# Optimization experiments

Measured on AMD Instinct MI355X. Metric: run time of the kernel, lower is better.

The kernel has to match this reference:

```python
import jax, jax.numpy as jnp
import numpy as np

B, N, D, OUT = 8, 2048, 128, 128

def setup_inputs() -> dict:
    key = jax.random.key(0)
    k1, k2, k3, k4 = jax.random.split(key, 4)
    input_ = jax.random.normal(k1, (B, N, D), dtype=jnp.float32)
    adj_matrix = jax.random.randint(k2, (B, N, N), 0, 2, dtype=jnp.int32)
    W = jax.random.normal(k3, (2 * D, OUT), dtype=jnp.float32) * 0.05
    b = jax.random.normal(k4, (OUT,), dtype=jnp.float32) * 0.05
    return {"input_": input_, "adj_matrix": adj_matrix, "W": W, "b": b}

def reference(input_, adj_matrix, W, b):
    adj = adj_matrix.astype(jnp.float32)           # [B,N,N]
    deg = jnp.sum(adj, axis=2)                     # [B,N]
    deg = jnp.where(deg == 0, 1.0, deg)
    agg = jnp.einsum('bnm,bmd->bnd', adj, input_) / deg[:, :, None]  # mean aggregation
    feat = jnp.concatenate([input_, agg], axis=2)  # [B,N,2D]
    out = jax.nn.sigmoid(feat @ W + b)             # [B,N,OUT]
    out = out / jnp.linalg.norm(out, axis=2, keepdims=True)
    return out
```

## Files before the change

kernel.cpp:

```cpp
#include <hip/hip_runtime.h>

#define Bn 8
#define Nn 2048
#define Dn 128
#define OUTn 128

typedef __attribute__((ext_vector_type(8))) short bf16x8;
typedef __attribute__((ext_vector_type(8))) unsigned short ushort8;
typedef __attribute__((ext_vector_type(4))) float f32x4;
typedef __attribute__((ext_vector_type(4))) int int4v;
typedef __attribute__((ext_vector_type(4))) float float4v;

__device__ __forceinline__ unsigned short f2bf(float f) {
  unsigned int u = __builtin_bit_cast(unsigned int, f);
  u += 0x7FFFu + ((u >> 16) & 1u);
  return (unsigned short)(u >> 16);
}

__global__ __launch_bounds__(256) void gcn_prep(const float* __restrict__ in,
                                                const float* __restrict__ W,
                                                unsigned short* __restrict__ inT,
                                                unsigned short* __restrict__ WT) {
  const int tid = threadIdx.x;
  if (blockIdx.x >= 256) {
    int gid = (blockIdx.x - 256) * 256 + tid;
    int j = gid >> 8, k = gid & 255;
    WT[gid] = f2bf(W[k * OUTn + j]);
    return;
  }
  const int b = blockIdx.x >> 5;
  const int n0 = (blockIdx.x & 31) * 64;
  __shared__ __attribute__((aligned(16))) unsigned short lds[64][130];
  #pragma unroll
  for (int c = 0; c < 32; ++c) {
    int e = tid + c * 256;
    int i = e >> 7, d = e & 127;
    lds[i][d] = f2bf(in[((size_t)(b * Nn + n0 + i)) * Dn + d]);
  }
  __syncthreads();
  #pragma unroll
  for (int c = 0; c < 4; ++c) {
    int ch = tid + c * 256;
    int d = ch >> 3, g = (ch & 7) * 8;
    ushort8 v;
    #pragma unroll
    for (int e = 0; e < 8; ++e) v[e] = lds[g + e][d];
    *(ushort8*)(inT + ((size_t)(b * Dn + d)) * Nn + n0 + g) = v;
  }
}

__global__ __launch_bounds__(256, 4) void gcn_main(
    const float* __restrict__ input_, const int* __restrict__ adj,
    const float* __restrict__ bvec, const unsigned short* __restrict__ inT,
    const unsigned short* __restrict__ WT, float* __restrict__ out) {
  constexpr int BM = 16, KB = 64, PAD = 8, NT = Nn / KB;
  __shared__ __attribute__((aligned(16))) unsigned short As[BM][KB + PAD];
  __shared__ __attribute__((aligned(16))) unsigned short Bs[Dn][KB + PAD];
  __shared__ __attribute__((aligned(16))) unsigned short aggl[BM][Dn + PAD];
  __shared__ float degs[BM];
  __shared__ float rowsum[BM][4];

  const int tid = threadIdx.x;
  const int w = tid >> 6;
  const int l = tid & 63;
  const int lr = l & 15, lg = l >> 4;

  const int wg = (blockIdx.x & 7) * 128 + (blockIdx.x >> 3);
  const int bb = wg >> 7;
  const int row0 = (wg & 127) * BM;

  const int ar = tid >> 4;
  const int ac = (tid & 15) * 4;
  const int* adj_row = adj + ((size_t)(bb * Nn + row0 + ar)) * Nn + ac;
  const unsigned short* inTb = inT + (size_t)bb * Dn * Nn;
  const int bd0 = tid >> 3;
  const int boff = (tid & 7) * 8;

  f32x4 acc[2] = {};
  int dsum = 0;
  int4v a_reg;
  ushort8 b_reg[4];

  a_reg = *(const int4v*)(adj_row);
  #pragma unroll
  for (int c = 0; c < 4; ++c)
    b_reg[c] = *(const ushort8*)(inTb + (size_t)(bd0 + c * 32) * Nn + boff);

  for (int kt = 0; kt < NT; ++kt) {
    if (kt) __syncthreads();
    {
      unsigned long long aw = 0;
      #pragma unroll
      for (int e = 0; e < 4; ++e) {
        int v = a_reg[e];
        dsum += (v != 0);
        if (v != 0) aw |= (0x3F80ull << (16 * e));
      }
      *(unsigned long long*)&As[ar][ac] = aw;
    }
    #pragma unroll
    for (int c = 0; c < 4; ++c)
      *(ushort8*)&Bs[bd0 + c * 32][boff] = b_reg[c];
    __syncthreads();
    if (kt + 1 < NT) {
      const int k0 = (kt + 1) * KB;
      a_reg = *(const int4v*)(adj_row + k0);
      #pragma unroll
      for (int c = 0; c < 4; ++c)
        b_reg[c] = *(const ushort8*)(inTb + (size_t)(bd0 + c * 32) * Nn + k0 + boff);
    }
    #pragma unroll
    for (int kc = 0; kc < 2; ++kc) {
      bf16x8 af = *(const bf16x8*)&As[lr][kc * 32 + lg * 8];
      #pragma unroll
      for (int cf = 0; cf < 2; ++cf) {
        bf16x8 bfm = *(const bf16x8*)&Bs[w * 32 + cf * 16 + lr][kc * 32 + lg * 8];
        acc[cf] = __builtin_amdgcn_mfma_f32_16x16x32_bf16(af, bfm, acc[cf], 0, 0, 0);
      }
    }
  }

  {
    int s = dsum;
    s += __shfl_down(s, 8);
    s += __shfl_down(s, 4);
    s += __shfl_down(s, 2);
    s += __shfl_down(s, 1);
    if ((tid & 15) == 0) {
      float fd = (float)s;
      degs[tid >> 4] = (fd == 0.0f) ? 1.0f : fd;
    }
  }
  __syncthreads();

  #pragma unroll
  for (int cf = 0; cf < 2; ++cf)
    #pragma unroll
    for (int reg = 0; reg < 4; ++reg) {
      int row = lg * 4 + reg;
      aggl[row][w * 32 + cf * 16 + lr] = f2bf(acc[cf][reg] / degs[row]);
    }
  __syncthreads();

  f32x4 acc2[2] = {};
  const float* xrow = input_ + ((size_t)(bb * Nn + row0 + lr)) * Dn;
  #pragma unroll
  for (int ks = 0; ks < 8; ++ks) {
    bf16x8 af;
    if (ks < 4) {
      float4v f0 = *(const float4v*)(xrow + ks * 32 + lg * 8);
      float4v f1 = *(const float4v*)(xrow + ks * 32 + lg * 8 + 4);
      ushort8 v;
      #pragma unroll
      for (int e = 0; e < 4; ++e) { v[e] = f2bf(f0[e]); v[e + 4] = f2bf(f1[e]); }
      af = __builtin_bit_cast(bf16x8, v);
    } else {
      af = *(const bf16x8*)&aggl[lr][(ks - 4) * 32 + lg * 8];
    }
    #pragma unroll
    for (int cf = 0; cf < 2; ++cf) {
      bf16x8 bw = *(const bf16x8*)(WT + (size_t)(w * 32 + cf * 16 + lr) * 256 +
                                   ks * 32 + lg * 8);
      acc2[cf] = __builtin_amdgcn_mfma_f32_16x16x32_bf16(af, bw, acc2[cf], 0, 0, 0);
    }
  }

  float bcol[2];
  bcol[0] = bvec[w * 32 + lr];
  bcol[1] = bvec[w * 32 + 16 + lr];
  float sg[2][4];
  #pragma unroll
  for (int cf = 0; cf < 2; ++cf)
    #pragma unroll
    for (int reg = 0; reg < 4; ++reg) {
      float x = acc2[cf][reg] + bcol[cf];
      sg[cf][reg] = 1.0f / (1.0f + expf(-x));
    }
  #pragma unroll
  for (int reg = 0; reg < 4; ++reg) {
    float p = sg[0][reg] * sg[0][reg] + sg[1][reg] * sg[1][reg];
    p += __shfl_xor(p, 1);
    p += __shfl_xor(p, 2);
    p += __shfl_xor(p, 4);
    p += __shfl_xor(p, 8);
    if (lr == 0) rowsum[lg * 4 + reg][w] = p;
  }
  __syncthreads();
  #pragma unroll
  for (int reg = 0; reg < 4; ++reg) {
    int row = lg * 4 + reg;
    float inv = rsqrtf(rowsum[row][0] + rowsum[row][1] + rowsum[row][2] + rowsum[row][3]);
    #pragma unroll
    for (int cf = 0; cf < 2; ++cf)
      out[((size_t)(bb * Nn + row0 + row)) * OUTn + w * 32 + cf * 16 + lr] =
          sg[cf][reg] * inv;
  }
}

extern "C" void kernel_launch(void* const* d_in, const int* in_sizes, int n_in,
                              void* d_out, int out_size, void* d_ws, size_t ws_size,
                              hipStream_t stream) {
  (void)in_sizes; (void)n_in; (void)out_size; (void)ws_size;
  const float* input_ = (const float*)d_in[0];
  const int* adj = (const int*)d_in[1];
  const float* W = (const float*)d_in[2];
  const float* bvec = (const float*)d_in[3];
  float* out = (float*)d_out;

  unsigned short* inT = (unsigned short*)d_ws;
  unsigned short* WT = inT + (size_t)Bn * Dn * Nn;

  hipLaunchKernelGGL(gcn_prep, dim3(384), dim3(256), 0, stream, input_, W, inT, WT);
  hipLaunchKernelGGL(gcn_main, dim3(1024), dim3(256), 0, stream, input_, adj, bvec, inT, WT, out);
}
```

Before: 52.72 us.

## Bit-pack adjacency in prep kernel and use larger 64-row tiles in main GEMM

The prep kernel now reads the int32 adjacency once, packs each row into 64-bit ballot masks and computes the degrees, writing both to workspace. The main kernel loads the packed bits and expands them into bf16 one/zero fragments in registers. It also switches to 64-row blocks of 512 threads with a double-buffered inT tile. With more output rows per block, each inT tile is reused across four times as many rows, so inT traffic drops. The adjacency is still read in full, now in prep, and the main kernel runs only 256 blocks, which risks lower occupancy and adds an extra bit-expansion step.

```diff
diff --git a/kernel.cpp b/kernel.cpp
--- a/kernel.cpp
+++ b/kernel.cpp
@@ -8,7 +8,6 @@
 typedef __attribute__((ext_vector_type(8))) short bf16x8;
 typedef __attribute__((ext_vector_type(8))) unsigned short ushort8;
 typedef __attribute__((ext_vector_type(4))) float f32x4;
-typedef __attribute__((ext_vector_type(4))) int int4v;
 typedef __attribute__((ext_vector_type(4))) float float4v;
 
 __device__ __forceinline__ unsigned short f2bf(float f) {
@@ -17,160 +16,183 @@
   return (unsigned short)(u >> 16);
 }
 
-__global__ __launch_bounds__(256) void gcn_prep(const float* __restrict__ in,
-                                                const float* __restrict__ W,
-                                                unsigned short* __restrict__ inT,
-                                                unsigned short* __restrict__ WT) {
+__global__ __launch_bounds__(256) void gcn_prep(
+    const float* __restrict__ in, const int* __restrict__ adj,
+    const float* __restrict__ W, unsigned long long* __restrict__ adjP,
+    float* __restrict__ deg, unsigned short* __restrict__ inT,
+    unsigned short* __restrict__ WT) {
+  __shared__ __attribute__((aligned(16))) unsigned short lds[64][130];
   const int tid = threadIdx.x;
-  if (blockIdx.x >= 256) {
-    int gid = (blockIdx.x - 256) * 256 + tid;
-    int j = gid >> 8, k = gid & 255;
-    WT[gid] = f2bf(W[k * OUTn + j]);
+  const int bid = blockIdx.x;
+
+  if (bid < 4096) {
+    const int wv = tid >> 6, l = tid & 63;
+    const int row = bid * 4 + wv;
+    const int* rp = adj + (size_t)row * Nn;
+    int v[32];
+    #pragma unroll
+    for (int k = 0; k < 32; ++k) v[k] = rp[k * 64 + l];
+    unsigned long long myw = 0;
+    int cnt = 0;
+    #pragma unroll
+    for (int k = 0; k < 32; ++k) {
+      unsigned long long w = __ballot(v[k] != 0);
+      cnt += __popcll(w);
+      if (l == k) myw = w;
+    }
+    if (l < 32) adjP[(size_t)row * 32 + l] = myw;
+    if (l == 0) deg[row] = (cnt == 0) ? 1.0f : (float)cnt;
     return;
   }
-  const int b = blockIdx.x >> 5;
-  const int n0 = (blockIdx.x & 31) * 64;
-  __shared__ __attribute__((aligned(16))) unsigned short lds[64][130];
-  #pragma unroll
-  for (int c = 0; c < 32; ++c) {
-    int e = tid + c * 256;
-    int i = e >> 7, d = e & 127;
-    lds[i][d] = f2bf(in[((size_t)(b * Nn + n0 + i)) * Dn + d]);
-  }
-  __syncthreads();
-  #pragma unroll
-  for (int c = 0; c < 4; ++c) {
-    int ch = tid + c * 256;
-    int d = ch >> 3, g = (ch & 7) * 8;
-    ushort8 v;
-    #pragma unroll
-    for (int e = 0; e < 8; ++e) v[e] = lds[g + e][d];
-    *(ushort8*)(inT + ((size_t)(b * Dn + d)) * Nn + n0 + g) = v;
-  }
-}
-
-__global__ __launch_bounds__(256, 4) void gcn_main(
-    const float* __restrict__ input_, const int* __restrict__ adj,
-    const float* __restrict__ bvec, const unsigned short* __restrict__ inT,
-    const unsigned short* __restrict__ WT, float* __restrict__ out) {
-  constexpr int BM = 16, KB = 64, PAD = 8, NT = Nn / KB;
-  __shared__ __attribute__((aligned(16))) unsigned short As[BM][KB + PAD];
-  __shared__ __attribute__((aligned(16))) unsigned short Bs[Dn][KB + PAD];
-  __shared__ __attribute__((aligned(16))) unsigned short aggl[BM][Dn + PAD];
-  __shared__ float degs[BM];
-  __shared__ float rowsum[BM][4];
-
+  if (bid < 4352) {
+    const int b = (bid - 4096) >> 5;
+    const int n0 = ((bid - 4096) & 31) * 64;
+    #pragma unroll
+    for (int c = 0; c < 32; ++c) {
+      int e = tid + c * 256;
+      int i = e >> 7, d = e & 127;
+      lds[i][d] = f2bf(in[((size_t)(b * Nn + n0 + i)) * Dn + d]);
+    }
+    __syncthreads();
+    #pragma unroll
+    for (int c = 0; c < 4; ++c) {
+      int ch = tid + c * 256;
+      int d = ch >> 3, g = (ch & 7) * 8;
+      ushort8 vv;
+      #pragma unroll
+      for (int e = 0; e < 8; ++e) vv[e] = lds[g + e][d];
+      *(ushort8*)(inT + ((size_t)(b * Dn + d)) * Nn + n0 + g) = vv;
+    }
+    return;
+  }
+  int gid = (bid - 4352) * 256 + tid;
+  int j = gid >> 8, k = gid & 255;
+  WT[gid] = f2bf(W[k * OUTn + j]);
+}
+
+union SMem {
+  struct {
+    unsigned long long A[64][33];
+    unsigned short Bs[2][128][72];
+  } g;
+  struct {
+    unsigned short aggl[64][136];
+    float rowsum[64][2];
+  } e;
+};
+
+__global__ __launch_bounds__(512, 2) void gcn_main(
+    const float* __restrict__ input_, const unsigned long long* __restrict__ adjP,
+    const float* __restrict__ deg, const float* __restrict__ bvec,
+    const unsigned short* __restrict__ inT, const unsigned short* __restrict__ WT,
+    float* __restrict__ out) {
+  __shared__ SMem sm;
   const int tid = threadIdx.x;
-  const int w = tid >> 6;
-  const int l = tid & 63;
-  const int lr = l & 15, lg = l >> 4;
-
-  const int wg = (blockIdx.x & 7) * 128 + (blockIdx.x >> 3);
-  const int bb = wg >> 7;
-  const int row0 = (wg & 127) * BM;
-
-  const int ar = tid >> 4;
-  const int ac = (tid & 15) * 4;
-  const int* adj_row = adj + ((size_t)(bb * Nn + row0 + ar)) * Nn + ac;
+  const int wv = tid >> 6;
+  const int l = tid & 63, lr = l & 15, lg = l >> 4;
+  const int rg = wv >> 1, chh = wv & 1;
+
+  const int swz = (blockIdx.x & 7) * 32 + (blockIdx.x >> 3);
+  const int bb = swz >> 5;
+  const int row0 = (swz & 31) * 64;
+  const int grow0 = bb * Nn + row0;
+
+  {
+    const int r = tid >> 3, w8 = (tid & 7) * 4;
+    const unsigned long long* src = adjP + (size_t)(grow0 + r) * 32 + w8;
+    #pragma unroll
+    for (int j = 0; j < 4; ++j) sm.g.A[r][w8 + j] = src[j];
+  }
+
   const unsigned short* inTb = inT + (size_t)bb * Dn * Nn;
-  const int bd0 = tid >> 3;
-  const int boff = (tid & 7) * 8;
-
-  f32x4 acc[2] = {};
-  int dsum = 0;
-  int4v a_reg;
-  ushort8 b_reg[4];
-
-  a_reg = *(const int4v*)(adj_row);
-  #pragma unroll
-  for (int c = 0; c < 4; ++c)
-    b_reg[c] = *(const ushort8*)(inTb + (size_t)(bd0 + c * 32) * Nn + boff);
-
-  for (int kt = 0; kt < NT; ++kt) {
-    if (kt) __syncthreads();
-    {
-      unsigned long long aw = 0;
-      #pragma unroll
-      for (int e = 0; e < 4; ++e) {
-        int v = a_reg[e];
-        dsum += (v != 0);
-        if (v != 0) aw |= (0x3F80ull << (16 * e));
-      }
-      *(unsigned long long*)&As[ar][ac] = aw;
-    }
-    #pragma unroll
-    for (int c = 0; c < 4; ++c)
-      *(ushort8*)&Bs[bd0 + c * 32][boff] = b_reg[c];
+  const int bd = tid >> 3;
+  const int koff = (tid & 7) * 8;
+
+  ushort8 breg[2][2];
+  #pragma unroll
+  for (int c = 0; c < 2; ++c)
+    breg[0][c] = *(const ushort8*)(inTb + (size_t)(bd + c * 64) * Nn + koff);
+  #pragma unroll
+  for (int c = 0; c < 2; ++c)
+    breg[1][c] = *(const ushort8*)(inTb + (size_t)(bd + c * 64) * Nn + 64 + koff);
+
+  f32x4 acc[4] = {};
+  const int arow = rg * 16 + lr;
+
+  #pragma unroll 2
+  for (int it = 0; it < 32; ++it) {
+    const int par = it & 1;
+    #pragma unroll
+    for (int c = 0; c < 2; ++c)
+      *(ushort8*)&sm.g.Bs[par][bd + c * 64][koff] = breg[par][c];
+    if (it + 2 < 32) {
+      #pragma unroll
+      for (int c = 0; c < 2; ++c)
+        breg[par][c] = *(const ushort8*)(inTb + (size_t)(bd + c * 64) * Nn +
+                                         (it + 2) * 64 + koff);
+    }
     __syncthreads();
-    if (kt + 1 < NT) {
-      const int k0 = (kt + 1) * KB;
-      a_reg = *(const int4v*)(adj_row + k0);
-      #pragma unroll
-      for (int c = 0; c < 4; ++c)
-        b_reg[c] = *(const ushort8*)(inTb + (size_t)(bd0 + c * 32) * Nn + k0 + boff);
-    }
-    #pragma unroll
-    for (int kc = 0; kc < 2; ++kc) {
-      bf16x8 af = *(const bf16x8*)&As[lr][kc * 32 + lg * 8];
-      #pragma unroll
-      for (int cf = 0; cf < 2; ++cf) {
-        bf16x8 bfm = *(const bf16x8*)&Bs[w * 32 + cf * 16 + lr][kc * 32 + lg * 8];
+    unsigned long long aw = sm.g.A[arow][it];
+    #pragma unroll
+    for (int kk = 0; kk < 2; ++kk) {
+      unsigned int bits = (unsigned int)(aw >> (kk * 32 + lg * 8)) & 0xFFu;
+      ushort8 av;
+      #pragma unroll
+      for (int e = 0; e < 8; ++e)
+        av[e] = (bits & (1u << e)) ? (unsigned short)0x3F80u : (unsigned short)0u;
+      bf16x8 af = __builtin_bit_cast(bf16x8, av);
+      #pragma unroll
+      for (int cf = 0; cf < 4; ++cf) {
+        bf16x8 bfm = *(const bf16x8*)&sm.g.Bs[par][chh * 64 + cf * 16 + lr]
+                                               [kk * 32 + lg * 8];
         acc[cf] = __builtin_amdgcn_mfma_f32_16x16x32_bf16(af, bfm, acc[cf], 0, 0, 0);
       }
     }
   }
 
-  {
-    int s = dsum;
-    s += __shfl_down(s, 8);
-    s += __shfl_down(s, 4);
-    s += __shfl_down(s, 2);
-    s += __shfl_down(s, 1);
-    if ((tid & 15) == 0) {
-      float fd = (float)s;
-      degs[tid >> 4] = (fd == 0.0f) ? 1.0f : fd;
-    }
-  }
   __syncthreads();
 
-  #pragma unroll
-  for (int cf = 0; cf < 2; ++cf)
-    #pragma unroll
-    for (int reg = 0; reg < 4; ++reg) {
-      int row = lg * 4 + reg;
-      aggl[row][w * 32 + cf * 16 + lr] = f2bf(acc[cf][reg] / degs[row]);
-    }
+  float dg[4];
+  #pragma unroll
+  for (int reg = 0; reg < 4; ++reg)
+    dg[reg] = deg[grow0 + rg * 16 + lg * 4 + reg];
+  #pragma unroll
+  for (int cf = 0; cf < 4; ++cf)
+    #pragma unroll
+    for (int reg = 0; reg < 4; ++reg)
+      sm.e.aggl[rg * 16 + lg * 4 + reg][chh * 64 + cf * 16 + lr] =
+          f2bf(acc[cf][reg] / dg[reg]);
   __syncthreads();
 
-  f32x4 acc2[2] = {};
-  const float* xrow = input_ + ((size_t)(bb * Nn + row0 + lr)) * Dn;
+  f32x4 acc2[4] = {};
+  const float* xrow = input_ + (size_t)(grow0 + rg * 16 + lr) * Dn;
   #pragma unroll
   for (int ks = 0; ks < 8; ++ks) {
     bf16x8 af;
     if (ks < 4) {
       float4v f0 = *(const float4v*)(xrow + ks * 32 + lg * 8);
       float4v f1 = *(const float4v*)(xrow + ks * 32 + lg * 8 + 4);
-      ushort8 v;
-      #pragma unroll
-      for (int e = 0; e < 4; ++e) { v[e] = f2bf(f0[e]); v[e + 4] = f2bf(f1[e]); }
-      af = __builtin_bit_cast(bf16x8, v);
+      ushort8 vv;
+      #pragma unroll
+      for (int e = 0; e < 4; ++e) { vv[e] = f2bf(f0[e]); vv[e + 4] = f2bf(f1[e]); }
+      af = __builtin_bit_cast(bf16x8, vv);
     } else {
-      af = *(const bf16x8*)&aggl[lr][(ks - 4) * 32 + lg * 8];
-    }
-    #pragma unroll
-    for (int cf = 0; cf < 2; ++cf) {
-      bf16x8 bw = *(const bf16x8*)(WT + (size_t)(w * 32 + cf * 16 + lr) * 256 +
+      af = *(const bf16x8*)&sm.e.aggl[rg * 16 + lr][(ks - 4) * 32 + lg * 8];
+    }
+    #pragma unroll
+    for (int cf = 0; cf < 4; ++cf) {
+      bf16x8 bw = *(const bf16x8*)(WT + (size_t)(chh * 64 + cf * 16 + lr) * 256 +
                                    ks * 32 + lg * 8);
       acc2[cf] = __builtin_amdgcn_mfma_f32_16x16x32_bf16(af, bw, acc2[cf], 0, 0, 0);
     }
   }
 
-  float bcol[2];
-  bcol[0] = bvec[w * 32 + lr];
-  bcol[1] = bvec[w * 32 + 16 + lr];
-  float sg[2][4];
-  #pragma unroll
-  for (int cf = 0; cf < 2; ++cf)
+  float bcol[4];
+  #pragma unroll
+  for (int cf = 0; cf < 4; ++cf) bcol[cf] = bvec[chh * 64 + cf * 16 + lr];
+  float sg[4][4];
+  #pragma unroll
+  for (int cf = 0; cf < 4; ++cf)
     #pragma unroll
     for (int reg = 0; reg < 4; ++reg) {
       float x = acc2[cf][reg] + bcol[cf];
@@ -178,21 +200,23 @@
     }
   #pragma unroll
   for (int reg = 0; reg < 4; ++reg) {
-    float p = sg[0][reg] * sg[0][reg] + sg[1][reg] * sg[1][reg];
+    float p = 0.f;
+    #pragma unroll
+    for (int cf = 0; cf < 4; ++cf) p += sg[cf][reg] * sg[cf][reg];
     p += __shfl_xor(p, 1);
     p += __shfl_xor(p, 2);
     p += __shfl_xor(p, 4);
     p += __shfl_xor(p, 8);
-    if (lr == 0) rowsum[lg * 4 + reg][w] = p;
+    if (lr == 0) sm.e.rowsum[rg * 16 + lg * 4 + reg][chh] = p;
   }
   __syncthreads();
   #pragma unroll
   for (int reg = 0; reg < 4; ++reg) {
-    int row = lg * 4 + reg;
-    float inv = rsqrtf(rowsum[row][0] + rowsum[row][1] + rowsum[row][2] + rowsum[row][3]);
-    #pragma unroll
-    for (int cf = 0; cf < 2; ++cf)
-      out[((size_t)(bb * Nn + row0 + row)) * OUTn + w * 32 + cf * 16 + lr] =
+    const int row = rg * 16 + lg * 4 + reg;
+    float inv = rsqrtf(sm.e.rowsum[row][0] + sm.e.rowsum[row][1]);
+    #pragma unroll
+    for (int cf = 0; cf < 4; ++cf)
+      out[(size_t)(grow0 + row) * OUTn + chh * 64 + cf * 16 + lr] =
           sg[cf][reg] * inv;
   }
 }
@@ -209,7 +233,12 @@
 
   unsigned short* inT = (unsigned short*)d_ws;
   unsigned short* WT = inT + (size_t)Bn * Dn * Nn;
-
-  hipLaunchKernelGGL(gcn_prep, dim3(384), dim3(256), 0, stream, input_, W, inT, WT);
-  hipLaunchKernelGGL(gcn_main, dim3(1024), dim3(256), 0, stream, input_, adj, bvec, inT, WT, out);
-}
+  unsigned long long* adjP =
+      (unsigned long long*)((char*)d_ws + 4194304 + 65536);
+  float* deg = (float*)((char*)d_ws + 4194304 + 65536 + 4194304);
+
+  hipLaunchKernelGGL(gcn_prep, dim3(4480), dim3(256), 0, stream,
+                     input_, adj, W, adjP, deg, inT, WT);
+  hipLaunchKernelGGL(gcn_main, dim3(256), dim3(512), 0, stream,
+                     input_, adjP, deg, bvec, inT, WT, out);
+}
```

Measured after the change: 67.24 us. 1.28x slower.

## Split aggregation K across waves, load operands directly to registers, reduce via LDS

Applied to the files above, without the earlier changes.

The adjacency GEMM is restructured so each wave handles a quarter of the K dimension (512 columns) and all 128 feature columns. The adj and transposed input fragments are loaded straight from global memory into MFMA registers with two-deep prefetch, which removes the per-tile LDS staging and the two barriers per K step. Partial sums from the four waves are then reduced through a shared buffer unioned with the epilogue storage. This raises per-thread accumulator registers (8 MFMA tiles) and uses strided, uncoalesced global loads of inT in place of cooperative LDS tiles.

```diff
diff --git a/kernel.cpp b/kernel.cpp
--- a/kernel.cpp
+++ b/kernel.cpp
@@ -49,125 +49,119 @@
   }
 }
 
+union EpiSMem {
+  float buf[4][16][136];
+  struct {
+    unsigned short aggl[16][136];
+    float rowsum[16][4];
+  } e;
+};
+
 __global__ __launch_bounds__(256, 4) void gcn_main(
     const float* __restrict__ input_, const int* __restrict__ adj,
     const float* __restrict__ bvec, const unsigned short* __restrict__ inT,
     const unsigned short* __restrict__ WT, float* __restrict__ out) {
-  constexpr int BM = 16, KB = 64, PAD = 8, NT = Nn / KB;
-  __shared__ __attribute__((aligned(16))) unsigned short As[BM][KB + PAD];
-  __shared__ __attribute__((aligned(16))) unsigned short Bs[Dn][KB + PAD];
-  __shared__ __attribute__((aligned(16))) unsigned short aggl[BM][Dn + PAD];
-  __shared__ float degs[BM];
-  __shared__ float rowsum[BM][4];
+  __shared__ EpiSMem sm;
+  __shared__ float degp[4][16];
 
   const int tid = threadIdx.x;
-  const int w = tid >> 6;
-  const int l = tid & 63;
-  const int lr = l & 15, lg = l >> 4;
-
-  const int wg = (blockIdx.x & 7) * 128 + (blockIdx.x >> 3);
-  const int bb = wg >> 7;
-  const int row0 = (wg & 127) * BM;
-
-  const int ar = tid >> 4;
-  const int ac = (tid & 15) * 4;
-  const int* adj_row = adj + ((size_t)(bb * Nn + row0 + ar)) * Nn + ac;
-  const unsigned short* inTb = inT + (size_t)bb * Dn * Nn;
-  const int bd0 = tid >> 3;
-  const int boff = (tid & 7) * 8;
-
-  f32x4 acc[2] = {};
+  const int wv = tid >> 6;
+  const int l = tid & 63, lr = l & 15, lg = l >> 4;
+
+  const int swz = (blockIdx.x & 7) * 128 + (blockIdx.x >> 3);
+  const int bb = swz >> 7;
+  const int row0 = (swz & 127) * 16;
+  const int grow0 = bb * Nn + row0;
+
+  const int* arow = adj + (size_t)(grow0 + lr) * Nn + wv * 512 + lg * 8;
+  const unsigned short* binT = inT + (size_t)bb * Dn * Nn + (size_t)lr * Nn +
+                               wv * 512 + lg * 8;
+
+  f32x4 acc[8] = {};
   int dsum = 0;
-  int4v a_reg;
-  ushort8 b_reg[4];
-
-  a_reg = *(const int4v*)(adj_row);
-  #pragma unroll
-  for (int c = 0; c < 4; ++c)
-    b_reg[c] = *(const ushort8*)(inTb + (size_t)(bd0 + c * 32) * Nn + boff);
-
-  for (int kt = 0; kt < NT; ++kt) {
-    if (kt) __syncthreads();
-    {
-      unsigned long long aw = 0;
-      #pragma unroll
-      for (int e = 0; e < 4; ++e) {
-        int v = a_reg[e];
-        dsum += (v != 0);
-        if (v != 0) aw |= (0x3F80ull << (16 * e));
-      }
-      *(unsigned long long*)&As[ar][ac] = aw;
-    }
-    #pragma unroll
-    for (int c = 0; c < 4; ++c)
-      *(ushort8*)&Bs[bd0 + c * 32][boff] = b_reg[c];
-    __syncthreads();
-    if (kt + 1 < NT) {
-      const int k0 = (kt + 1) * KB;
-      a_reg = *(const int4v*)(adj_row + k0);
-      #pragma unroll
-      for (int c = 0; c < 4; ++c)
-        b_reg[c] = *(const ushort8*)(inTb + (size_t)(bd0 + c * 32) * Nn + k0 + boff);
-    }
-    #pragma unroll
-    for (int kc = 0; kc < 2; ++kc) {
-      bf16x8 af = *(const bf16x8*)&As[lr][kc * 32 + lg * 8];
-      #pragma unroll
-      for (int cf = 0; cf < 2; ++cf) {
-        bf16x8 bfm = *(const bf16x8*)&Bs[w * 32 + cf * 16 + lr][kc * 32 + lg * 8];
-        acc[cf] = __builtin_amdgcn_mfma_f32_16x16x32_bf16(af, bfm, acc[cf], 0, 0, 0);
-      }
-    }
-  }
-
+
+  int4v aCur0 = *(const int4v*)(arow);
+  int4v aCur1 = *(const int4v*)(arow + 4);
+  int4v aNxt0 = *(const int4v*)(arow + 32);
+  int4v aNxt1 = *(const int4v*)(arow + 36);
+
+  #pragma unroll
+  for (int it = 0; it < 16; ++it) {
+    ushort8 av;
+    #pragma unroll
+    for (int e = 0; e < 4; ++e) {
+      int v0 = aCur0[e], v1 = aCur1[e];
+      dsum += (v0 != 0) + (v1 != 0);
+      av[e]     = (v0 != 0) ? (unsigned short)0x3F80u : (unsigned short)0u;
+      av[e + 4] = (v1 != 0) ? (unsigned short)0x3F80u : (unsigned short)0u;
+    }
+    bf16x8 af = __builtin_bit_cast(bf16x8, av);
+    aCur0 = aNxt0; aCur1 = aNxt1;
+    if (it + 2 < 16) {
+      aNxt0 = *(const int4v*)(arow + (it + 2) * 32);
+      aNxt1 = *(const int4v*)(arow + (it + 2) * 32 + 4);
+    }
+    #pragma unroll
+    for (int cf = 0; cf < 8; ++cf) {
+      bf16x8 bfm = *(const bf16x8*)(binT + (size_t)cf * 16 * Nn + it * 32);
+      acc[cf] = __builtin_amdgcn_mfma_f32_16x16x32_bf16(af, bfm, acc[cf], 0, 0, 0);
+    }
+  }
+
+  #pragma unroll
+  for (int cf = 0; cf < 8; ++cf)
+    #pragma unroll
+    for (int reg = 0; reg < 4; ++reg)
+      sm.buf[wv][lg * 4 + reg][cf * 16 + lr] = acc[cf][reg];
   {
     int s = dsum;
-    s += __shfl_down(s, 8);
-    s += __shfl_down(s, 4);
-    s += __shfl_down(s, 2);
-    s += __shfl_down(s, 1);
-    if ((tid & 15) == 0) {
-      float fd = (float)s;
-      degs[tid >> 4] = (fd == 0.0f) ? 1.0f : fd;
-    }
-  }
-  __syncthreads();
-
-  #pragma unroll
-  for (int cf = 0; cf < 2; ++cf)
-    #pragma unroll
-    for (int reg = 0; reg < 4; ++reg) {
-      int row = lg * 4 + reg;
-      aggl[row][w * 32 + cf * 16 + lr] = f2bf(acc[cf][reg] / degs[row]);
-    }
+    s += __shfl_xor(s, 16);
+    s += __shfl_xor(s, 32);
+    if (l < 16) degp[wv][lr] = (float)s;
+  }
+  __syncthreads();
+
+  const int row = tid >> 4, c0 = (tid & 15) * 8;
+  float dg = degp[0][row] + degp[1][row] + degp[2][row] + degp[3][row];
+  if (dg == 0.f) dg = 1.f;
+  const float inv = 1.f / dg;
+  ushort8 packed;
+  #pragma unroll
+  for (int e = 0; e < 8; ++e) {
+    float ssum = sm.buf[0][row][c0 + e] + sm.buf[1][row][c0 + e] +
+                 sm.buf[2][row][c0 + e] + sm.buf[3][row][c0 + e];
+    packed[e] = f2bf(ssum * inv);
+  }
+  __syncthreads();
+  *(ushort8*)&sm.e.aggl[row][c0] = packed;
   __syncthreads();
 
   f32x4 acc2[2] = {};
-  const float* xrow = input_ + ((size_t)(bb * Nn + row0 + lr)) * Dn;
+  const float* xrow = input_ + (size_t)(grow0 + lr) * Dn;
   #pragma unroll
   for (int ks = 0; ks < 8; ++ks) {
     bf16x8 af;
     if (ks < 4) {
       float4v f0 = *(const float4v*)(xrow + ks * 32 + lg * 8);
       float4v f1 = *(const float4v*)(xrow + ks * 32 + lg * 8 + 4);
-      ushort8 v;
+      ushort8 vv;
       #pragma unroll
-      for (int e = 0; e < 4; ++e) { v[e] = f2bf(f0[e]); v[e + 4] = f2bf(f1[e]); }
-      af = __builtin_bit_cast(bf16x8, v);
+      for (int e = 0; e < 4; ++e) { vv[e] = f2bf(f0[e]); vv[e + 4] = f2bf(f1[e]); }
+      af = __builtin_bit_cast(bf16x8, vv);
     } else {
-      af = *(const bf16x8*)&aggl[lr][(ks - 4) * 32 + lg * 8];
+      af = *(const bf16x8*)&sm.e.aggl[lr][(ks - 4) * 32 + lg * 8];
     }
     #pragma unroll
     for (int cf = 0; cf < 2; ++cf) {
-      bf16x8 bw = *(const bf16x8*)(WT + (size_t)(w * 32 + cf * 16 + lr) * 256 +
+      bf16x8 bw = *(const bf16x8*)(WT + (size_t)(wv * 32 + cf * 16 + lr) * 256 +
                                    ks * 32 + lg * 8);
       acc2[cf] = __builtin_amdgcn_mfma_f32_16x16x32_bf16(af, bw, acc2[cf], 0, 0, 0);
     }
   }
 
   float bcol[2];
-  bcol[0] = bvec[w * 32 + lr];
-  bcol[1] = bvec[w * 32 + 16 + lr];
+  bcol[0] = bvec[wv * 32 + lr];
+  bcol[1] = bvec[wv * 32 + 16 + lr];
   float sg[2][4];
   #pragma unroll
   for (int cf = 0; cf < 2; ++cf)
@@ -183,17 +177,18 @@
     p += __shfl_xor(p, 2);
     p += __shfl_xor(p, 4);
     p += __shfl_xor(p, 8);
-    if (lr == 0) rowsum[lg * 4 + reg][w] = p;
+    if (lr == 0) sm.e.rowsum[lg * 4 + reg][wv] = p;
   }
   __syncthreads();
   #pragma unroll
   for (int reg = 0; reg < 4; ++reg) {
-    int row = lg * 4 + reg;
-    float inv = rsqrtf(rowsum[row][0] + rowsum[row][1] + rowsum[row][2] + rowsum[row][3]);
+    const int r2 = lg * 4 + reg;
+    float nrm = rsqrtf(sm.e.rowsum[r2][0] + sm.e.rowsum[r2][1] +
+                       sm.e.rowsum[r2][2] + sm.e.rowsum[r2][3]);
     #pragma unroll
     for (int cf = 0; cf < 2; ++cf)
-      out[((size_t)(bb * Nn + row0 + row)) * OUTn + w * 32 + cf * 16 + lr] =
-          sg[cf][reg] * inv;
+      out[(size_t)(grow0 + r2) * OUTn + wv * 32 + cf * 16 + lr] =
+          sg[cf][reg] * nrm;
   }
 }
 
@@ -211,5 +206,6 @@
   unsigned short* WT = inT + (size_t)Bn * Dn * Nn;
 
   hipLaunchKernelGGL(gcn_prep, dim3(384), dim3(256), 0, stream, input_, W, inT, WT);
-  hipLaunchKernelGGL(gcn_main, dim3(1024), dim3(256), 0, stream, input_, adj, bvec, inT, WT, out);
-}
+  hipLaunchKernelGGL(gcn_main, dim3(1024), dim3(256), 0, stream,
+                     input_, adj, bvec, inT, WT, out);
+}
```

New measurement: 95.36 us. +80.9%, slower.
